# Performance work log

Hardware: AMD Instinct MI355X
Metric: run time of the kernel (lower is better)

## Reference

```python
import jax, jax.numpy as jnp
import numpy as np

N, C, H, E = 100000, 128, 8, 600000
HD = C // H
EPS = 1e-5


def _layernorm(x, g, b):
    mu = jnp.mean(x, axis=-1, keepdims=True)
    var = jnp.var(x, axis=-1, keepdims=True)
    return (x - mu) * jax.lax.rsqrt(var + EPS) * g + b


def setup_inputs() -> dict:
    key = jax.random.key(0)
    ks = jax.random.split(key, 12)
    s = 1.0 / np.sqrt(C)
    x = jax.random.normal(ks[0], (N, C), dtype=jnp.float32)
    edge_index = jax.random.randint(ks[1], (2, E), 0, N, dtype=jnp.int64)
    # linear weights stored [in, out]
    Wq = jax.random.normal(ks[2], (C, C), jnp.float32) * s
    Wk = jax.random.normal(ks[3], (C, C), jnp.float32) * s
    Wv = jax.random.normal(ks[4], (C, C), jnp.float32) * s
    Wo = jax.random.normal(ks[5], (C, C), jnp.float32) * s
    W1 = jax.random.normal(ks[6], (C, 4 * C), jnp.float32) * s
    W2 = jax.random.normal(ks[7], (4 * C, C), jnp.float32) * (1.0 / np.sqrt(4 * C))
    return {
        'x': x, 'edge_index': edge_index,
        'Wq': Wq, 'bq': jnp.zeros((C,), jnp.float32),
        'Wk': Wk, 'bk': jnp.zeros((C,), jnp.float32),
        'Wv': Wv, 'bv': jnp.zeros((C,), jnp.float32),
        'Wo': Wo, 'bo': jnp.zeros((C,), jnp.float32),
        'W1': W1, 'b1': jnp.zeros((4 * C,), jnp.float32),
        'W2': W2, 'b2': jnp.zeros((C,), jnp.float32),
        'g1': jnp.ones((C,), jnp.float32), 'beta1': jnp.zeros((C,), jnp.float32),
        'g2': jnp.ones((C,), jnp.float32), 'beta2': jnp.zeros((C,), jnp.float32),
    }


def reference(x, edge_index, Wq, bq, Wk, bk, Wv, bv, Wo, bo,
              W1, b1, W2, b2, g1, beta1, g2, beta2):
    src = edge_index[0]  # x_j (source nodes)
    dst = edge_index[1]  # x_i (target nodes, aggregation index)

    residual = x
    h = _layernorm(x, g1, beta1)

    # project at node level, then gather per edge (same math as per-edge proj)
    Q = h @ Wq + bq  # [N, C]
    K = h @ Wk + bk
    V = h @ Wv + bv

    q = Q[dst].reshape(E, H, HD)
    k = K[src].reshape(E, H, HD)
    v = V[src].reshape(E, H, HD)

    attn = jnp.sum(q * k, axis=-1) / np.sqrt(HD)  # [E, H]
    attn = jax.nn.softmax(attn, axis=-1)          # softmax over heads (per source)
    msg = (v * attn[..., None]).reshape(E, C)     # [E, C]

    aggr = jax.ops.segment_sum(msg, dst, num_segments=N)  # [N, C]
    out = aggr @ Wo + bo
    x = out + residual

    residual = x
    h = _layernorm(x, g2, beta2)
    h = jax.nn.relu(h @ W1 + b1) @ W2 + b2
    return h + residual
```

## Files before the change

### kernel.cpp

```cpp
#include <hip/hip_runtime.h>
#include <hip/hip_bf16.h>

#define C_DIM 128
#define EPS_LN 1e-5f

typedef short bf16x8 __attribute__((ext_vector_type(8)));
typedef float f32x4  __attribute__((ext_vector_type(4)));
typedef __hip_bfloat16 bf16;

__device__ inline unsigned short f2bu(float f) {
    bf16 h = __float2bfloat16(f);
    return *reinterpret_cast<unsigned short*>(&h);
}
__device__ inline float blo(unsigned int u) { return __uint_as_float(u << 16); }
__device__ inline float bhi(unsigned int u) { return __uint_as_float(u & 0xffff0000u); }
__device__ inline ushort4 pack4(float a, float b, float c, float d) {
    ushort4 r; r.x = f2bu(a); r.y = f2bu(b); r.z = f2bu(c); r.w = f2bu(d); return r;
}

__device__ inline void async_copy16(const bf16* g, bf16* s) {
    __builtin_amdgcn_global_load_lds(
        (const __attribute__((address_space(1))) unsigned int*)g,
        (__attribute__((address_space(3))) unsigned int*)s,
        16, 0, 0);
}

__global__ __launch_bounds__(256) void wconv_all(
    const float* __restrict__ Wq, const float* __restrict__ Wk,
    const float* __restrict__ Wv, const float* __restrict__ Wo,
    const float* __restrict__ W1, const float* __restrict__ W2,
    const float* __restrict__ bq, const float* __restrict__ bk,
    const float* __restrict__ bv, bf16* __restrict__ dst) {
    int idx = blockIdx.x * 256 + threadIdx.x;
    if (idx < 65536) {
        int r = idx >> 14, o = idx & 16383;
        int k = o >> 7, nn = o & 127;
        const float* W = (r == 0) ? Wq : (r == 1) ? Wk : (r == 2) ? Wv : Wo;
        dst[(r << 14) + nn * 128 + k] = __float2bfloat16(W[o]);
    } else if (idx < 131072) {
        int o = idx - 65536;
        int k = o >> 9, nn = o & 511;
        dst[65536 + nn * 128 + k] = __float2bfloat16(W1[o]);
    } else if (idx < 196608) {
        int o = idx - 131072;
        int k = o >> 7, nn = o & 127;
        dst[131072 + nn * 512 + k] = __float2bfloat16(W2[o]);
    } else if (idx < 196992) {
        int j = idx - 196608;
        int grp = j >> 7, col = j & 127;
        const float* bp = (grp == 0) ? bq : (grp == 1) ? bk : bv;
        ((float*)(dst + 196608))[j] = bp[col];
    }
}

__global__ __launch_bounds__(256) void zeroi_kernel(int* __restrict__ p, int n) {
    int i = blockIdx.x * 256 + threadIdx.x;
    if (i < n) p[i] = 0;
}

__global__ __launch_bounds__(256) void ln_kernel(
    const float* __restrict__ x, const float* __restrict__ g,
    const float* __restrict__ b, bf16* __restrict__ out, int n) {
    int wave = threadIdx.x >> 6;
    int lane = threadIdx.x & 63;
    int row = blockIdx.x * 4 + wave;
    if (row >= n) return;
    float2 v = ((const float2*)(x + (size_t)row * C_DIM))[lane];
    float s  = v.x + v.y;
    float ss = v.x * v.x + v.y * v.y;
    #pragma unroll
    for (int o = 1; o < 64; o <<= 1) {
        s  += __shfl_xor(s, o);
        ss += __shfl_xor(ss, o);
    }
    float mu  = s * (1.0f / C_DIM);
    float var = ss * (1.0f / C_DIM) - mu * mu;
    float rs  = rsqrtf(var + EPS_LN);
    float2 gg = ((const float2*)g)[lane];
    float2 bb = ((const float2*)b)[lane];
    __hip_bfloat162 o2;
    o2.x = __float2bfloat16((v.x - mu) * rs * gg.x + bb.x);
    o2.y = __float2bfloat16((v.y - mu) * rs * gg.y + bb.y);
    ((__hip_bfloat162*)(out + (size_t)row * C_DIM))[lane] = o2;
}

template<bool OUTBF16, bool RELU, bool FUSE_LN, int KSTEPS>
__global__ __launch_bounds__(256) void gemm_lds(
    const bf16* __restrict__ A, int lda,
    const bf16* __restrict__ Bt, int Kfull,
    const float* __restrict__ biasBase,
    void* __restrict__ Cd, int ldc, size_t obStride,
    const float* __restrict__ resid, int ldres,
    int M,
    const float* __restrict__ g, const float* __restrict__ be,
    bf16* __restrict__ h2) {
    __shared__ bf16 As[128][128];
    __shared__ bf16 Bs[128][128];
    int tid  = threadIdx.x;
    int lane = tid & 63;
    int w    = tid >> 6;
    int m = lane & 15, q = lane >> 4;
    int row0 = blockIdx.x * 128;
    const bf16* Bbase = Bt + (size_t)blockIdx.y * 128 * Kfull;

    f32x4 acc[2][8];
    #pragma unroll
    for (int rt = 0; rt < 2; rt++)
        #pragma unroll
        for (int ct = 0; ct < 8; ct++) acc[rt][ct] = (f32x4){0.f, 0.f, 0.f, 0.f};

    int rsub  = lane >> 4;
    int cslot = lane & 15;

    for (int kt = 0; kt < KSTEPS; kt++) {
        #pragma unroll
        for (int i = 0; i < 8; i++) {
            int arow = w * 32 + i * 4 + rsub;
            int scol = (cslot ^ (arow & 7)) << 3;
            int garow = row0 + arow;
            if (garow > M - 1) garow = M - 1;
            async_copy16(A + (size_t)garow * lda + kt * 128 + scol, &As[w * 32 + i * 4][0]);
            async_copy16(Bbase + (size_t)arow * Kfull + kt * 128 + scol, &Bs[w * 32 + i * 4][0]);
        }
        __syncthreads();
        #pragma unroll
        for (int ks = 0; ks < 4; ks++) {
            int sofs = ((ks * 4 + q) ^ (m & 7)) << 3;
            bf16x8 af0 = *(const bf16x8*)&As[w * 32 + m][sofs];
            bf16x8 af1 = *(const bf16x8*)&As[w * 32 + 16 + m][sofs];
            #pragma unroll
            for (int ct = 0; ct < 8; ct++) {
                bf16x8 bf = *(const bf16x8*)&Bs[ct * 16 + m][sofs];
                acc[0][ct] = __builtin_amdgcn_mfma_f32_16x16x32_bf16(bf, af0, acc[0][ct], 0, 0, 0);
                acc[1][ct] = __builtin_amdgcn_mfma_f32_16x16x32_bf16(bf, af1, acc[1][ct], 0, 0, 0);
            }
        }
        if (kt + 1 < KSTEPS) __syncthreads();
    }

    #pragma unroll
    for (int rt = 0; rt < 2; rt++) {
        int row = row0 + w * 32 + rt * 16 + m;
        bool valid = row < M;
        float vals[8][4];
        #pragma unroll
        for (int ct = 0; ct < 8; ct++) {
            int col = ct * 16 + q * 4;
            float4 bv = make_float4(0.f, 0.f, 0.f, 0.f);
            if (biasBase) bv = *(const float4*)(biasBase + blockIdx.y * 128 + col);
            float4 rv = make_float4(0.f, 0.f, 0.f, 0.f);
            if (resid && valid) rv = *(const float4*)(resid + (size_t)row * ldres + col);
            vals[ct][0] = acc[rt][ct][0] + bv.x + rv.x;
            vals[ct][1] = acc[rt][ct][1] + bv.y + rv.y;
            vals[ct][2] = acc[rt][ct][2] + bv.z + rv.z;
            vals[ct][3] = acc[rt][ct][3] + bv.w + rv.w;
        }
        if (FUSE_LN) {
            float s1 = 0.f, s2 = 0.f;
            #pragma unroll
            for (int ct = 0; ct < 8; ct++)
                #pragma unroll
                for (int r = 0; r < 4; r++) { s1 += vals[ct][r]; s2 += vals[ct][r] * vals[ct][r]; }
            s1 += __shfl_xor(s1, 16); s1 += __shfl_xor(s1, 32);
            s2 += __shfl_xor(s2, 16); s2 += __shfl_xor(s2, 32);
            float mu  = s1 * (1.0f / 128.f);
            float var = s2 * (1.0f / 128.f) - mu * mu;
            float rs  = rsqrtf(var + EPS_LN);
            if (valid) {
                #pragma unroll
                for (int ct = 0; ct < 8; ct++) {
                    int col = ct * 16 + q * 4;
                    *(float4*)((float*)Cd + (size_t)row * ldc + col) =
                        make_float4(vals[ct][0], vals[ct][1], vals[ct][2], vals[ct][3]);
                    float4 gg = *(const float4*)(g + col);
                    float4 bb = *(const float4*)(be + col);
                    *(ushort4*)(h2 + (size_t)row * 128 + col) =
                        pack4((vals[ct][0] - mu) * rs * gg.x + bb.x,
                              (vals[ct][1] - mu) * rs * gg.y + bb.y,
                              (vals[ct][2] - mu) * rs * gg.z + bb.z,
                              (vals[ct][3] - mu) * rs * gg.w + bb.w);
                }
            }
        } else if (valid) {
            #pragma unroll
            for (int ct = 0; ct < 8; ct++) {
                int col = ct * 16 + q * 4;
                float v0 = vals[ct][0], v1 = vals[ct][1];
                float v2 = vals[ct][2], v3 = vals[ct][3];
                if (RELU) {
                    v0 = fmaxf(v0, 0.f); v1 = fmaxf(v1, 0.f);
                    v2 = fmaxf(v2, 0.f); v3 = fmaxf(v3, 0.f);
                }
                if (OUTBF16) {
                    *(ushort4*)((bf16*)Cd + blockIdx.y * obStride + (size_t)row * ldc + col) =
                        pack4(v0, v1, v2, v3);
                } else {
                    *(float4*)((float*)Cd + blockIdx.y * obStride + (size_t)row * ldc + col) =
                        make_float4(v0, v1, v2, v3);
                }
            }
        }
    }
}

__global__ __launch_bounds__(256) void hist_kernel(
    const int* __restrict__ eidx, int* __restrict__ deg, int E_) {
    int e = blockIdx.x * 256 + threadIdx.x;
    if (e >= E_) return;
    atomicAdd(&deg[eidx[E_ + e]], 1);
}

__global__ __launch_bounds__(256) void alloc_kernel(
    const int* __restrict__ deg, int* __restrict__ start,
    int* __restrict__ cursor, int* __restrict__ counter, int n) {
    int i = blockIdx.x * 256 + threadIdx.x;
    if (i >= n) return;
    int d = deg[i];
    int s = atomicAdd(counter, d);
    start[i] = s;
    cursor[i] = s;
}

__global__ __launch_bounds__(256) void scatter_kernel(
    const int* __restrict__ eidx, int* __restrict__ cursor,
    int* __restrict__ esrc, int E_) {
    int e = blockIdx.x * 256 + threadIdx.x;
    if (e >= E_) return;
    int src = eidx[e];
    int dst = eidx[E_ + e];
    int pos = atomicAdd(&cursor[dst], 1);
    esrc[pos] = src;
}

__global__ __launch_bounds__(256) void attn_aggr_kernel(
    const bf16* __restrict__ Q, const bf16* __restrict__ K,
    const bf16* __restrict__ V,
    const int* __restrict__ start, const int* __restrict__ deg,
    const int* __restrict__ esrc, bf16* __restrict__ ag, int n) {
    int wave = threadIdx.x >> 6;
    int lane = threadIdx.x & 63;
    int i = blockIdx.x * 4 + wave;
    if (i >= n) return;
    int s = start[i], d = deg[i];
    unsigned qu = ((const unsigned*)(Q + (size_t)i * 128))[lane];
    float qx = blo(qu), qy = bhi(qu);
    float ax = 0.f, ay = 0.f;
    int j = s, e_ = s + d;
    for (; j + 2 <= e_; j += 2) {
        int s0 = esrc[j], s1 = esrc[j + 1];
        unsigned k0 = ((const unsigned*)(K + (size_t)s0 * 128))[lane];
        unsigned k1 = ((const unsigned*)(K + (size_t)s1 * 128))[lane];
        unsigned v0 = ((const unsigned*)(V + (size_t)s0 * 128))[lane];
        unsigned v1 = ((const unsigned*)(V + (size_t)s1 * 128))[lane];
        float p0 = qx * blo(k0) + qy * bhi(k0);
        float p1 = qx * blo(k1) + qy * bhi(k1);
        p0 += __shfl_xor(p0, 1); p1 += __shfl_xor(p1, 1);
        p0 += __shfl_xor(p0, 2); p1 += __shfl_xor(p1, 2);
        p0 += __shfl_xor(p0, 4); p1 += __shfl_xor(p1, 4);
        p0 *= 0.25f; p1 *= 0.25f;
        float m0 = fmaxf(p0, __shfl_xor(p0, 8));
        float m1 = fmaxf(p1, __shfl_xor(p1, 8));
        m0 = fmaxf(m0, __shfl_xor(m0, 16)); m1 = fmaxf(m1, __shfl_xor(m1, 16));
        m0 = fmaxf(m0, __shfl_xor(m0, 32)); m1 = fmaxf(m1, __shfl_xor(m1, 32));
        float e0 = expf(p0 - m0), e1 = expf(p1 - m1);
        float t0 = e0 + __shfl_xor(e0, 8);
        float t1 = e1 + __shfl_xor(e1, 8);
        t0 += __shfl_xor(t0, 16); t1 += __shfl_xor(t1, 16);
        t0 += __shfl_xor(t0, 32); t1 += __shfl_xor(t1, 32);
        float a0 = e0 / t0, a1 = e1 / t1;
        ax += a0 * blo(v0) + a1 * blo(v1);
        ay += a0 * bhi(v0) + a1 * bhi(v1);
    }
    if (j < e_) {
        int s0 = esrc[j];
        unsigned k0 = ((const unsigned*)(K + (size_t)s0 * 128))[lane];
        unsigned v0 = ((const unsigned*)(V + (size_t)s0 * 128))[lane];
        float p0 = qx * blo(k0) + qy * bhi(k0);
        p0 += __shfl_xor(p0, 1);
        p0 += __shfl_xor(p0, 2);
        p0 += __shfl_xor(p0, 4);
        p0 *= 0.25f;
        float m0 = fmaxf(p0, __shfl_xor(p0, 8));
        m0 = fmaxf(m0, __shfl_xor(m0, 16));
        m0 = fmaxf(m0, __shfl_xor(m0, 32));
        float e0 = expf(p0 - m0);
        float t0 = e0 + __shfl_xor(e0, 8);
        t0 += __shfl_xor(t0, 16);
        t0 += __shfl_xor(t0, 32);
        float a0 = e0 / t0;
        ax += a0 * blo(v0);
        ay += a0 * bhi(v0);
    }
    __hip_bfloat162 o2;
    o2.x = __float2bfloat16(ax);
    o2.y = __float2bfloat16(ay);
    ((__hip_bfloat162*)(ag + (size_t)i * 128))[lane] = o2;
}

extern "C" void kernel_launch(void* const* d_in, const int* in_sizes, int n_in,
                              void* d_out, int out_size, void* d_ws, size_t ws_size,
                              hipStream_t stream) {
    const float* x   = (const float*)d_in[0];
    const int*  eidx = (const int*)d_in[1];
    const float* Wq = (const float*)d_in[2];  const float* bq = (const float*)d_in[3];
    const float* Wk = (const float*)d_in[4];  const float* bk = (const float*)d_in[5];
    const float* Wv = (const float*)d_in[6];  const float* bv = (const float*)d_in[7];
    const float* Wo = (const float*)d_in[8];  const float* bo = (const float*)d_in[9];
    const float* W1 = (const float*)d_in[10]; const float* b1 = (const float*)d_in[11];
    const float* W2 = (const float*)d_in[12]; const float* b2 = (const float*)d_in[13];
    const float* g1 = (const float*)d_in[14]; const float* be1 = (const float*)d_in[15];
    const float* g2 = (const float*)d_in[16]; const float* be2 = (const float*)d_in[17];
    float* out = (float*)d_out;

    int n  = in_sizes[0] / C_DIM;
    int E_ = in_sizes[1] / 2;
    size_t nf = (size_t)n * 128;

    bf16* Wt    = (bf16*)d_ws;
    float* bqkv = (float*)(Wt + 196608);
    bf16* reg0  = (bf16*)(bqkv + 384);
    bf16* h1 = reg0;
    bf16* Qb = reg0 + nf;
    bf16* Kb = reg0 + 2 * nf;
    bf16* Vb = reg0 + 3 * nf;
    bf16* uB = reg0;
    bf16* ag = reg0 + 4 * nf;
    char* r2 = (char*)(ag + nf);
    int*  esrc   = (int*)r2;
    int*  ideg   = esrc + E_;
    int*  counter = ideg + n;
    int*  istart  = ideg + n + 1;
    int*  icursor = istart + n;
    bf16* h2 = (bf16*)r2;

    dim3 b256(256);
    dim3 lnGrid((n + 3) / 4);
    int rb = (n + 127) / 128;
    dim3 eGrid((E_ + 255) / 256);
    dim3 nGrid((n + 255) / 256);
    dim3 n1Grid((n + 1 + 255) / 256);
    dim3 n4Grid((n + 3) / 4);

    wconv_all<<<dim3(770), b256, 0, stream>>>(Wq, Wk, Wv, Wo, W1, W2, bq, bk, bv, Wt);
    zeroi_kernel<<<n1Grid, b256, 0, stream>>>(ideg, n + 1);
    ln_kernel<<<lnGrid, b256, 0, stream>>>(x, g1, be1, h1, n);
    gemm_lds<true, false, false, 1><<<dim3(rb, 3), b256, 0, stream>>>(
        h1, 128, Wt, 128, bqkv, Qb, 128, nf, nullptr, 0, n, nullptr, nullptr, nullptr);
    hist_kernel<<<eGrid, b256, 0, stream>>>(eidx, ideg, E_);
    alloc_kernel<<<nGrid, b256, 0, stream>>>(ideg, istart, icursor, counter, n);
    scatter_kernel<<<eGrid, b256, 0, stream>>>(eidx, icursor, esrc, E_);
    attn_aggr_kernel<<<n4Grid, b256, 0, stream>>>(Qb, Kb, Vb, istart, ideg, esrc, ag, n);
    gemm_lds<false, false, true, 1><<<dim3(rb, 1), b256, 0, stream>>>(
        ag, 128, Wt + 49152, 128, bo, out, 128, 0, x, 128, n, g2, be2, h2);
    gemm_lds<true, true, false, 1><<<dim3(rb, 4), b256, 0, stream>>>(
        h2, 128, Wt + 65536, 128, b1, uB, 512, 128, nullptr, 0, n, nullptr, nullptr, nullptr);
    gemm_lds<false, false, false, 4><<<dim3(rb, 1), b256, 0, stream>>>(
        uB, 512, Wt + 131072, 512, b2, out, 128, 0, out, 128, n, nullptr, nullptr, nullptr);
}
```

Before: 468.0 us.

## Batch 8 edges per wave in attention score computation with head-per-lane layout

Reworks the per-node attention aggregation so each wave handles 8 edges at once. Each 8-lane group owns one edge and each lane one head, doing a full 16-element dot product from 32-byte K loads. This cuts the cross-lane shuffle reductions per edge and allows more K loads in flight. Softmax weights and source indices are then broadcast by shuffle for a per-edge V accumulation. It also switches to exp2f with a folded log2e scale and a fast division, and partial batches clamp the index and recompute the last edge's score.

```diff
diff --git a/kernel.cpp b/kernel.cpp
--- a/kernel.cpp
+++ b/kernel.cpp
@@ -232,6 +232,13 @@
     esrc[pos] = src;
 }
 
+__device__ inline float dot8f(uint4 a, uint4 b) {
+    return blo(a.x) * blo(b.x) + bhi(a.x) * bhi(b.x)
+         + blo(a.y) * blo(b.y) + bhi(a.y) * bhi(b.y)
+         + blo(a.z) * blo(b.z) + bhi(a.z) * bhi(b.z)
+         + blo(a.w) * blo(b.w) + bhi(a.w) * bhi(b.w);
+}
+
 __global__ __launch_bounds__(256) void attn_aggr_kernel(
     const bf16* __restrict__ Q, const bf16* __restrict__ K,
     const bf16* __restrict__ V,
@@ -242,54 +249,36 @@
     int i = blockIdx.x * 4 + wave;
     if (i >= n) return;
     int s = start[i], d = deg[i];
-    unsigned qu = ((const unsigned*)(Q + (size_t)i * 128))[lane];
-    float qx = blo(qu), qy = bhi(qu);
+    int end = s + d;
+    int g = lane >> 3;
+    int l = lane & 7;
+    const uint4* qh = (const uint4*)(Q + (size_t)i * 128 + l * 16);
+    uint4 q0 = qh[0], q1 = qh[1];
+    const float SC = 0.25f * 1.44269504089f;
     float ax = 0.f, ay = 0.f;
-    int j = s, e_ = s + d;
-    for (; j + 2 <= e_; j += 2) {
-        int s0 = esrc[j], s1 = esrc[j + 1];
-        unsigned k0 = ((const unsigned*)(K + (size_t)s0 * 128))[lane];
-        unsigned k1 = ((const unsigned*)(K + (size_t)s1 * 128))[lane];
-        unsigned v0 = ((const unsigned*)(V + (size_t)s0 * 128))[lane];
-        unsigned v1 = ((const unsigned*)(V + (size_t)s1 * 128))[lane];
-        float p0 = qx * blo(k0) + qy * bhi(k0);
-        float p1 = qx * blo(k1) + qy * bhi(k1);
-        p0 += __shfl_xor(p0, 1); p1 += __shfl_xor(p1, 1);
-        p0 += __shfl_xor(p0, 2); p1 += __shfl_xor(p1, 2);
-        p0 += __shfl_xor(p0, 4); p1 += __shfl_xor(p1, 4);
-        p0 *= 0.25f; p1 *= 0.25f;
-        float m0 = fmaxf(p0, __shfl_xor(p0, 8));
-        float m1 = fmaxf(p1, __shfl_xor(p1, 8));
-        m0 = fmaxf(m0, __shfl_xor(m0, 16)); m1 = fmaxf(m1, __shfl_xor(m1, 16));
-        m0 = fmaxf(m0, __shfl_xor(m0, 32)); m1 = fmaxf(m1, __shfl_xor(m1, 32));
-        float e0 = expf(p0 - m0), e1 = expf(p1 - m1);
-        float t0 = e0 + __shfl_xor(e0, 8);
-        float t1 = e1 + __shfl_xor(e1, 8);
-        t0 += __shfl_xor(t0, 16); t1 += __shfl_xor(t1, 16);
-        t0 += __shfl_xor(t0, 32); t1 += __shfl_xor(t1, 32);
-        float a0 = e0 / t0, a1 = e1 / t1;
-        ax += a0 * blo(v0) + a1 * blo(v1);
-        ay += a0 * bhi(v0) + a1 * bhi(v1);
-    }
-    if (j < e_) {
-        int s0 = esrc[j];
-        unsigned k0 = ((const unsigned*)(K + (size_t)s0 * 128))[lane];
-        unsigned v0 = ((const unsigned*)(V + (size_t)s0 * 128))[lane];
-        float p0 = qx * blo(k0) + qy * bhi(k0);
-        p0 += __shfl_xor(p0, 1);
-        p0 += __shfl_xor(p0, 2);
-        p0 += __shfl_xor(p0, 4);
-        p0 *= 0.25f;
-        float m0 = fmaxf(p0, __shfl_xor(p0, 8));
-        m0 = fmaxf(m0, __shfl_xor(m0, 16));
-        m0 = fmaxf(m0, __shfl_xor(m0, 32));
-        float e0 = expf(p0 - m0);
-        float t0 = e0 + __shfl_xor(e0, 8);
-        t0 += __shfl_xor(t0, 16);
-        t0 += __shfl_xor(t0, 32);
-        float a0 = e0 / t0;
-        ax += a0 * blo(v0);
-        ay += a0 * bhi(v0);
+    for (int j = s; j < end; j += 8) {
+        int eg = j + g;
+        int se = esrc[eg < end ? eg : end - 1];
+        const uint4* kh = (const uint4*)(K + (size_t)se * 128 + l * 16);
+        uint4 k0 = kh[0], k1 = kh[1];
+        float p = (dot8f(q0, k0) + dot8f(q1, k1)) * SC;
+        float mx = fmaxf(p, __shfl_xor(p, 1));
+        mx = fmaxf(mx, __shfl_xor(mx, 2));
+        mx = fmaxf(mx, __shfl_xor(mx, 4));
+        float ex = exp2f(p - mx);
+        float t = ex + __shfl_xor(ex, 1);
+        t += __shfl_xor(t, 2);
+        t += __shfl_xor(t, 4);
+        float wgt = __fdividef(ex, t);
+        #pragma unroll
+        for (int e = 0; e < 8; e++) {
+            if (j + e >= end) break;
+            float we = __shfl(wgt, e * 8 + (lane >> 3));
+            int sv = __shfl(se, e * 8);
+            unsigned vu = ((const unsigned*)(V + (size_t)sv * 128))[lane];
+            ax += we * blo(vu);
+            ay += we * bhi(vu);
+        }
     }
     __hip_bfloat162 o2;
     o2.x = __float2bfloat16(ax);
```

Measured after the change: 462.7 us. No clear change (-1.1%).
